# Kernel optimization log

Hardware: AMD Instinct MI355X
Metric: run time of the kernel (lower is better)

The kernel has to match this reference:

```python
import jax, jax.numpy as jnp
import numpy as np

N = 8192          # number of gaussians
N_SH = 4          # circular harmonic order -> 2*N_SH+1 coefficients
H, W = 1024, 1024 # raster resolution
P = 48            # per-gaussian splat footprint (pixels), covers +/- 24 px
S_MIN = 1.0 / 30.0    # 1 / n_gaussian_max_pixels  (inverse std, pixels^-1)
S_MAX = 1.0 / 0.75    # 1 / n_gaussian_min_pixels
MU_BORDER = 1.05
EPS = 1e-6


def setup_inputs() -> dict:
    key = jax.random.key(0)
    k1, k2, k3, k4, k5 = jax.random.split(key, 5)
    xyz = jax.random.uniform(k1, (N, 2), dtype=jnp.float32) * 2 - 1
    features = jax.random.uniform(k2, (N, 2 * N_SH + 1, 3), dtype=jnp.float32)
    opacity = 0.1 + 0.9 * jax.random.uniform(k3, (N,), dtype=jnp.float32)
    scaling = jax.random.uniform(k4, (N, 2), dtype=jnp.float32)
    rotation = jax.random.uniform(k5, (N,), dtype=jnp.float32)
    return {"xyz": xyz, "features": features, "opacity": opacity,
            "scaling": scaling, "rotation": rotation}


def _sh2d(theta_n, shcoef_nmc):
    # circular harmonics basis: [1, sin(t), cos(t), sin(2t), cos(2t), ...]
    basis = [jnp.ones_like(theta_n)]
    for i in range(N_SH):
        basis.append(jnp.sin(theta_n * (i + 1)))
        basis.append(jnp.cos(theta_n * (i + 1)))
    b_nm = jnp.stack(basis, axis=-1)                 # [N, 2*N_SH+1]
    return jnp.einsum('nm,nmc->nc', b_nm, shcoef_nmc)  # [N, 3]


def reference(xyz, features, opacity, scaling, rotation):
    # --- parameter activations (mirror module properties) ---
    mu = jnp.clip(xyz, -1.0, 1.0) * MU_BORDER                      # [N,2] in NDC
    S = jnp.clip(scaling, 0.0, 1.0) * (S_MAX - S_MIN) + S_MIN      # [N,2] inverse stds (1/px)
    angle = jnp.remainder(rotation, 1.0) * (2.0 * jnp.pi)          # [N]
    op = jnp.clip(opacity, 0.0, 1.0)                               # [N]
    rgb = _sh2d(angle, features)                                   # [N,3]

    # --- per-gaussian local pixel footprint ---
    res = jnp.array([W - 1, H - 1], dtype=mu.dtype)
    mu_pix = (mu + 1.0) * 0.5 * res                                # [N,2] (x,y) in pixels
    base = jnp.floor(mu_pix).astype(jnp.int32)                     # [N,2]
    offs = jnp.arange(P, dtype=jnp.int32) - P // 2                 # [P]
    px = base[:, 0, None, None] + offs[None, None, :]              # [N,P,P] (x varies last)
    py = base[:, 1, None, None] + offs[None, :, None]              # [N,P,P]
    dx = px.astype(mu.dtype) - mu_pix[:, 0, None, None]            # [N,P,P]
    dy = py.astype(mu.dtype) - mu_pix[:, 1, None, None]

    # rotate offset into gaussian frame: v = diag(S) @ R(angle)^T @ d
    c = jnp.cos(angle)[:, None, None]
    s = jnp.sin(angle)[:, None, None]
    rx = c * dx + s * dy
    ry = -s * dx + c * dy
    vx = S[:, 0, None, None] * rx
    vy = S[:, 1, None, None] * ry
    w = op[:, None, None] * jnp.exp(-0.5 * (vx * vx + vy * vy))    # [N,P,P]

    valid = (px >= 0) & (px < W) & (py >= 0) & (py < H)
    w = jnp.where(valid, w, 0.0)

    # --- scatter-accumulate onto framebuffer ---
    idx = (jnp.clip(py, 0, H - 1) * W + jnp.clip(px, 0, W - 1)).reshape(-1)  # [N*P*P]
    wf = w.reshape(-1)                                                        # [N*P*P]
    contrib = (w[..., None] * rgb[:, None, None, :]).reshape(-1, 3)           # [N*P*P,3]

    rgb_acc = jnp.zeros((H * W, 3), dtype=w.dtype).at[idx].add(contrib)
    w_acc = jnp.zeros((H * W,), dtype=w.dtype).at[idx].add(wf)
    img = rgb_acc / (w_acc[:, None] + EPS)
    return img.reshape(H, W, 3)
```

## Files before the change

### kernel.cpp

```cpp
#include <hip/hip_runtime.h>

#define NG   8192
#define NSH  4
#define HH   1024
#define WW   1024
#define PP   48
#define TILE 16
#define TX   (WW / TILE)
#define TY   (HH / TILE)
#define NTILES (TX * TY)
#define CAP  128
#define S_MIN (1.0f / 30.0f)
#define S_MAX (1.0f / 0.75f)
#define TWO_PI 6.28318530717958647692f
#define AEXP 0.8493218002880191f


__global__ void prep_kernel(const float* __restrict__ xyz,
                            const float* __restrict__ feat,
                            const float* __restrict__ opac,
                            const float* __restrict__ scal,
                            const float* __restrict__ rot,
                            int* __restrict__ counts,
                            unsigned* __restrict__ ranges,
                            float4* __restrict__ params) {
    int g = blockIdx.x * blockDim.x + threadIdx.x;
    if (g < NTILES) counts[g] = 0;
    if (g >= NG) return;

    float mx = fminf(fmaxf(xyz[2 * g + 0], -1.0f), 1.0f) * 1.05f;
    float my = fminf(fmaxf(xyz[2 * g + 1], -1.0f), 1.0f) * 1.05f;
    float s0 = fminf(fmaxf(scal[2 * g + 0], 0.0f), 1.0f) * (S_MAX - S_MIN) + S_MIN;
    float s1 = fminf(fmaxf(scal[2 * g + 1], 0.0f), 1.0f) * (S_MAX - S_MIN) + S_MIN;
    float rr = rot[g];
    float ang = (rr - floorf(rr)) * TWO_PI;
    float op = fminf(fmaxf(opac[g], 0.0f), 1.0f);

    float c, s;
    __sincosf(ang, &s, &c);

    const float* f = feat + g * (2 * NSH + 1) * 3;
    float r = f[0], gg = f[1], b = f[2];
    float sk = s, ck = c;
    #pragma unroll
    for (int i = 1; i <= NSH; ++i) {
        int ms = (2 * i - 1) * 3, mc = (2 * i) * 3;
        r  += sk * f[ms + 0] + ck * f[mc + 0];
        gg += sk * f[ms + 1] + ck * f[mc + 1];
        b  += sk * f[ms + 2] + ck * f[mc + 2];
        float sn = sk * c + ck * s;
        float cn = ck * c - sk * s;
        sk = sn; ck = cn;
    }

    float mu_px = (mx + 1.0f) * 0.5f * (float)(WW - 1);
    float mu_py = (my + 1.0f) * 0.5f * (float)(HH - 1);
    int bx = (int)floorf(mu_px), by = (int)floorf(mu_py);

    float a0 = AEXP * s0, a1 = AEXP * s1;
    params[3 * g + 0] = make_float4(mu_px, mu_py, a0 * c, a0 * s);
    params[3 * g + 1] = make_float4(-a1 * s, a1 * c, op, r);
    params[3 * g + 2] = make_float4(gg, b, __int_as_float(bx), __int_as_float(by));

    int x0 = bx - PP / 2, x1 = bx + PP / 2 - 1;
    int y0 = by - PP / 2, y1 = by + PP / 2 - 1;
    unsigned pack = 0;
    if (!(x1 < 0 || x0 > WW - 1 || y1 < 0 || y0 > HH - 1)) {
        int tx0 = max(x0, 0) / TILE, tx1 = min(x1, WW - 1) / TILE;
        int ty0 = max(y0, 0) / TILE, ty1 = min(y1, HH - 1) / TILE;
        pack = (unsigned)tx0 | ((unsigned)ty0 << 8)
             | ((unsigned)(tx1 - tx0 + 1) << 16) | ((unsigned)(ty1 - ty0 + 1) << 20);
    }
    ranges[g] = pack;
}

__global__ void bin_kernel(const unsigned* __restrict__ ranges,
                           int* __restrict__ counts,
                           int* __restrict__ list) {
    int t = blockIdx.x * blockDim.x + threadIdx.x;
    int g = t >> 4, slot = t & 15;
    unsigned rng = ranges[g];
    int nx = (rng >> 16) & 0xF, ny = (rng >> 20) & 0xF;
    int sx = slot & 3, sy = slot >> 2;
    if (sx >= nx || sy >= ny) return;
    int tx = (int)(rng & 0xFF) + sx;
    int ty = (int)((rng >> 8) & 0xFF) + sy;
    int tile = ty * TX + tx;
    int pos = atomicAdd(&counts[tile], 1);
    if (pos < CAP) list[tile * CAP + pos] = g;
}

__global__ void __launch_bounds__(256)
render_kernel(const int* __restrict__ counts,
              const int* __restrict__ list,
              const float4* __restrict__ params,
              float* __restrict__ out) {
    int tile = blockIdx.x;
    int tx = tile & (TX - 1), ty = tile / TX;
    int lx = threadIdx.x & (TILE - 1), ly = threadIdx.x / TILE;
    int px = tx * TILE + lx, py = ty * TILE + ly;
    float fpx = (float)px, fpy = (float)py;

    int n = min(counts[tile], CAP);

    __shared__ float4 sp[3 * CAP];
    for (int i = threadIdx.x; i < 3 * n; i += 256) {
        int gi = list[tile * CAP + i / 3];
        sp[i] = params[3 * gi + i % 3];
    }
    __syncthreads();

    float fr = 0.f, fg = 0.f, fb = 0.f, fw = 0.f;

    for (int j = 0; j < n; ++j) {
        float4 e0 = sp[3 * j + 0];
        float4 e1 = sp[3 * j + 1];
        float4 e2 = sp[3 * j + 2];
        int bx = __float_as_int(e2.z);
        int by = __float_as_int(e2.w);
        unsigned ox = (unsigned)(px - bx + PP / 2);
        unsigned oy = (unsigned)(py - by + PP / 2);
        if ((ox < PP) & (oy < PP)) {
            float dx = fpx - e0.x;
            float dy = fpy - e0.y;
            float vx = e0.z * dx + e0.w * dy;
            float vy = e1.x * dx + e1.y * dy;
            float t = fmaf(vx, vx, vy * vy);
            float w = e1.z * exp2f(-t);
            fr += w * e1.w;
            fg += w * e2.x;
            fb += w * e2.y;
            fw += w;
        }
    }

    float inv = 1.0f / (fw + 1e-6f);
    int idx = py * WW + px;
    out[3 * idx + 0] = fr * inv;
    out[3 * idx + 1] = fg * inv;
    out[3 * idx + 2] = fb * inv;
}

extern "C" void kernel_launch(void* const* d_in, const int* in_sizes, int n_in,
                              void* d_out, int out_size, void* d_ws, size_t ws_size,
                              hipStream_t stream) {
    const float* xyz  = (const float*)d_in[0];
    const float* feat = (const float*)d_in[1];
    const float* opac = (const float*)d_in[2];
    const float* scal = (const float*)d_in[3];
    const float* rot  = (const float*)d_in[4];
    float* out = (float*)d_out;

    char* ws = (char*)d_ws;
    size_t off = 0;
    int*      counts = (int*)(ws + off);      off += (size_t)NTILES * sizeof(int);
    unsigned* ranges = (unsigned*)(ws + off); off += (size_t)NG * sizeof(unsigned);
    float4*   params = (float4*)(ws + off);   off += (size_t)NG * 3 * sizeof(float4);
    int*      list   = (int*)(ws + off);

    prep_kernel<<<NG / 256, 256, 0, stream>>>(xyz, feat, opac, scal, rot,
                                              counts, ranges, params);
    bin_kernel<<<NG * 16 / 256, 256, 0, stream>>>(ranges, counts, list);
    render_kernel<<<NTILES, 256, 0, stream>>>(counts, list, params, out);
}
```

Measured before the change: 92.92 us.

## Register-block render so each thread shades four rows with one wave per tile

The render kernel now uses 64 threads per 16x16 tile, and each thread accumulates four pixels spaced four rows apart. Each thread does one shared-memory fetch, one x-footprint test and one base projection per gaussian, then reuses them for its four rows through incremental FMAs. This cuts LDS traffic and per-pixel overhead, and exp2f is replaced with the AMDGCN hardware exp2 builtin. The prep kernel also moves to 64-thread blocks. The trade-off is fewer threads per tile and more registers per thread, which reduces latency hiding within each block.

After: 88.18 us. -5.1%, faster.

```diff
diff --git a/kernel.cpp b/kernel.cpp
--- a/kernel.cpp
+++ b/kernel.cpp
@@ -15,15 +15,22 @@
 #define TWO_PI 6.28318530717958647692f
 #define AEXP 0.8493218002880191f
 
+#if __has_builtin(__builtin_amdgcn_exp2f)
+#define EXP2F(x) __builtin_amdgcn_exp2f(x)
+#else
+#define EXP2F(x) exp2f(x)
+#endif
 
-__global__ void prep_kernel(const float* __restrict__ xyz,
-                            const float* __restrict__ feat,
-                            const float* __restrict__ opac,
-                            const float* __restrict__ scal,
-                            const float* __restrict__ rot,
-                            int* __restrict__ counts,
-                            unsigned* __restrict__ ranges,
-                            float4* __restrict__ params) {
+
+__global__ void __launch_bounds__(64)
+prep_kernel(const float* __restrict__ xyz,
+            const float* __restrict__ feat,
+            const float* __restrict__ opac,
+            const float* __restrict__ scal,
+            const float* __restrict__ rot,
+            int* __restrict__ counts,
+            unsigned* __restrict__ ranges,
+            float4* __restrict__ params) {
     int g = blockIdx.x * blockDim.x + threadIdx.x;
     if (g < NTILES) counts[g] = 0;
     if (g >= NG) return;
@@ -90,27 +97,32 @@
     if (pos < CAP) list[tile * CAP + pos] = g;
 }
 
-__global__ void __launch_bounds__(256)
+__global__ void __launch_bounds__(64)
 render_kernel(const int* __restrict__ counts,
               const int* __restrict__ list,
               const float4* __restrict__ params,
               float* __restrict__ out) {
     int tile = blockIdx.x;
     int tx = tile & (TX - 1), ty = tile / TX;
-    int lx = threadIdx.x & (TILE - 1), ly = threadIdx.x / TILE;
-    int px = tx * TILE + lx, py = ty * TILE + ly;
-    float fpx = (float)px, fpy = (float)py;
+    int lx = threadIdx.x & (TILE - 1), ly0 = threadIdx.x >> 4;
+    int px = tx * TILE + lx, py0 = ty * TILE + ly0;
+    float fpx = (float)px, fpy0 = (float)py0;
 
     int n = min(counts[tile], CAP);
 
     __shared__ float4 sp[3 * CAP];
-    for (int i = threadIdx.x; i < 3 * n; i += 256) {
-        int gi = list[tile * CAP + i / 3];
-        sp[i] = params[3 * gi + i % 3];
+    for (int e = threadIdx.x; e < n; e += 64) {
+        int gi = list[tile * CAP + e];
+        sp[3 * e + 0] = params[3 * gi + 0];
+        sp[3 * e + 1] = params[3 * gi + 1];
+        sp[3 * e + 2] = params[3 * gi + 2];
     }
     __syncthreads();
 
-    float fr = 0.f, fg = 0.f, fb = 0.f, fw = 0.f;
+    float fr[4] = {0.f, 0.f, 0.f, 0.f};
+    float fg[4] = {0.f, 0.f, 0.f, 0.f};
+    float fb[4] = {0.f, 0.f, 0.f, 0.f};
+    float fw[4] = {0.f, 0.f, 0.f, 0.f};
 
     for (int j = 0; j < n; ++j) {
         float4 e0 = sp[3 * j + 0];
@@ -119,26 +131,36 @@
         int bx = __float_as_int(e2.z);
         int by = __float_as_int(e2.w);
         unsigned ox = (unsigned)(px - bx + PP / 2);
-        unsigned oy = (unsigned)(py - by + PP / 2);
-        if ((ox < PP) & (oy < PP)) {
+        if (ox < PP) {
+            unsigned oy0 = (unsigned)(py0 - by + PP / 2);
             float dx = fpx - e0.x;
-            float dy = fpy - e0.y;
-            float vx = e0.z * dx + e0.w * dy;
-            float vy = e1.x * dx + e1.y * dy;
-            float t = fmaf(vx, vx, vy * vy);
-            float w = e1.z * exp2f(-t);
-            fr += w * e1.w;
-            fg += w * e2.x;
-            fb += w * e2.y;
-            fw += w;
+            float dy0 = fpy0 - e0.y;
+            float vx0 = e0.z * dx + e0.w * dy0;
+            float vy0 = e1.x * dx + e1.y * dy0;
+            #pragma unroll
+            for (int k = 0; k < 4; ++k) {
+                if (oy0 + 4u * k < PP) {
+                    float fk = 4.0f * (float)k;
+                    float vx = fmaf(fk, e0.w, vx0);
+                    float vy = fmaf(fk, e1.y, vy0);
+                    float w = e1.z * EXP2F(-fmaf(vx, vx, vy * vy));
+                    fr[k] += w * e1.w;
+                    fg[k] += w * e2.x;
+                    fb[k] += w * e2.y;
+                    fw[k] += w;
+                }
+            }
         }
     }
 
-    float inv = 1.0f / (fw + 1e-6f);
-    int idx = py * WW + px;
-    out[3 * idx + 0] = fr * inv;
-    out[3 * idx + 1] = fg * inv;
-    out[3 * idx + 2] = fb * inv;
+    #pragma unroll
+    for (int k = 0; k < 4; ++k) {
+        float inv = 1.0f / (fw[k] + 1e-6f);
+        int idx = (py0 + 4 * k) * WW + px;
+        out[3 * idx + 0] = fr[k] * inv;
+        out[3 * idx + 1] = fg[k] * inv;
+        out[3 * idx + 2] = fb[k] * inv;
+    }
 }
 
 extern "C" void kernel_launch(void* const* d_in, const int* in_sizes, int n_in,
@@ -158,8 +180,8 @@
     float4*   params = (float4*)(ws + off);   off += (size_t)NG * 3 * sizeof(float4);
     int*      list   = (int*)(ws + off);
 
-    prep_kernel<<<NG / 256, 256, 0, stream>>>(xyz, feat, opac, scal, rot,
-                                              counts, ranges, params);
+    prep_kernel<<<NG / 64, 64, 0, stream>>>(xyz, feat, opac, scal, rot,
+                                            counts, ranges, params);
     bin_kernel<<<NG * 16 / 256, 256, 0, stream>>>(ranges, counts, list);
-    render_kernel<<<NTILES, 256, 0, stream>>>(counts, list, params, out);
+    render_kernel<<<NTILES, 64, 0, stream>>>(counts, list, params, out);
 }
```
